# Kernel optimization log

Hardware: AMD Instinct MI355X
Metric: run time of the kernel (lower is better)

Reference implementation:

```python
import jax, jax.numpy as jnp
import numpy as np


def sparse_conv3d(images, kernel, default_value, base_plane, dilations=(1, 1, 1)):
    """Sparse 3D conv over a per-pixel base-plane-aligned volume.

    images:     [B, H, W, D, C]  local depth slabs per pixel
    kernel:     [kh, kw, kd, C, F]
    base_plane: [B, H, W, 1] int  global depth offset of slab start per pixel
    Neighbor sample at pixel (h', w') and local depth d uses that neighbor's
    local index d + od + base_plane[h,w] - base_plane[h',w']; out-of-range
    (spatial or depth) samples are filled with default_value.
    """
    B, H, W, D, C = images.shape
    kh, kw, kd, _, F = kernel.shape
    d0, d1, d2 = dilations
    bp = base_plane[..., 0].astype(jnp.int32)  # [B,H,W]
    hs = jnp.arange(H)
    ws = jnp.arange(W)
    ds = jnp.arange(D)
    dv = jnp.asarray(default_value, images.dtype).reshape(())
    out = jnp.zeros((B, H, W, D, F), images.dtype)
    for i in range(kh):
        oh = (i - kh // 2) * d0
        h_idx = hs + oh
        valid_h = (h_idx >= 0) & (h_idx < H)
        h_c = jnp.clip(h_idx, 0, H - 1)
        for j in range(kw):
            ow = (j - kw // 2) * d1
            w_idx = ws + ow
            valid_w = (w_idx >= 0) & (w_idx < W)
            w_c = jnp.clip(w_idx, 0, W - 1)
            # gather shifted neighbor slabs and their base offsets
            img_n = images[:, h_c][:, :, w_c]      # [B,H,W,D,C]
            bp_n = bp[:, h_c][:, :, w_c]            # [B,H,W]
            rel = (bp - bp_n)[..., None]            # depth realignment [B,H,W,1]
            sp_valid = (valid_h[None, :, None, None] & valid_w[None, None, :, None])
            for k in range(kd):
                od = (k - kd // 2) * d2
                d_idx = ds[None, None, None, :] + od + rel  # [B,H,W,D]
                valid = sp_valid & (d_idx >= 0) & (d_idx < D)
                d_c = jnp.clip(d_idx, 0, D - 1)
                vals = jnp.take_along_axis(img_n, d_c[..., None], axis=3)  # [B,H,W,D,C]
                vals = jnp.where(valid[..., None], vals, dv)
                out = out + jnp.einsum('bhwdc,cf->bhwdf', vals, kernel[i, j, k])
    return out


def setup_inputs() -> dict:
    key = jax.random.key(0)
    k1, k2, k3 = jax.random.split(key, 3)
    B, H, W, D, C, F = 2, 96, 128, 32, 16, 16
    images = jax.random.normal(k1, (B, H, W, D, C), dtype=jnp.float32)
    base_plane = jax.random.randint(k2, (B, H, W, 1), 0, 8, dtype=jnp.int32)
    kernel = jax.random.normal(k3, (3, 3, 3, C, F), dtype=jnp.float32) * 0.05
    default_value = jnp.zeros((1,), dtype=jnp.float32)
    return {"images": images, "base_plane": base_plane, "kernel": kernel,
            "default_value": default_value}


def reference(images, base_plane, kernel, default_value):
    return sparse_conv3d(images, kernel, default_value[0], base_plane, dilations=(1, 1, 1))
```

## Files before the change

### kernel.cpp

```cpp
#include <hip/hip_runtime.h>
#include <hip/hip_bf16.h>

typedef __attribute__((ext_vector_type(8))) short short8;
typedef __attribute__((ext_vector_type(4))) short s16x4;
typedef __attribute__((ext_vector_type(4))) float f32x4;
typedef __attribute__((ext_vector_type(4))) int i32x4;

#define NB_H 96
#define NB_W 128
#define NB_D 32
#define NB_C 16
#define NB_F 16
#define NPIX (2 * NB_H * NB_W)
#define KB2_U16 (14 * 512)
#define WS_NEED ((size_t)KB2_U16 * 2)
#define SLAB_STRIDE 1280
#define NSLAB 36
#define DV_OFF (NSLAB * SLAB_STRIDE)
#define KB_OFF (DV_OFF + 64)
#define LDS_BYTES (KB_OFF + KB2_U16 * 2)

static __device__ __forceinline__ short fcvt(float f) {
  return (short)__builtin_bit_cast(unsigned short, __float2bfloat16(f));
}


__global__ __launch_bounds__(256) void sconv3d_wprep(
    const float* __restrict__ kern, unsigned short* __restrict__ kb2) {
  const int i = blockIdx.x * 256 + threadIdx.x;
  if (i >= KB2_U16) return;
  const int p = i >> 9;
  const int g = (i >> 7) & 3;
  const int f = (i >> 3) & 15;
  const int j = i & 7;
  const int k = g * 8 + j;
  int lo, hi;
  if (p < 12) {
    const int q = p / 3, m = p % 3;
    lo = (m == 0) ? 6 * q : (m == 1) ? 6 * q + 3 : 6 * q + 2;
    hi = (m == 0) ? 6 * q + 1 : (m == 1) ? 6 * q + 4 : 6 * q + 5;
  } else if (p == 12) { lo = 24; hi = 25; }
  else { lo = 26; hi = -1; }
  const int t = (k < 16) ? lo : hi;
  const int c = k & 15;
  kb2[i] = (t >= 0) ? (unsigned short)fcvt(kern[(t * 16 + c) * 16 + f])
                    : (unsigned short)0;
}

__global__ __launch_bounds__(512, 4) void sconv3d_fused3(
    const float* __restrict__ img, const int* __restrict__ bp,
    const unsigned short* __restrict__ kb2, const float* __restrict__ dvp,
    float* __restrict__ out) {
  __shared__ char Sb[LDS_BYTES];
  const int tid = threadIdx.x;
  const int lane = tid & 63;
  const int r = lane & 15;
  const int grp = lane >> 4;
  const int vc = (grp & 1) * 16;
  const int halfbit = grp >> 1;
  const int rA = r + halfbit - 1;
  const int rX = r + 1;
  const int voff_dv = DV_OFF + vc;

  {
    const i32x4* src = (const i32x4*)kb2;
    i32x4* dst = (i32x4*)(Sb + KB_OFF);
    for (int i = tid; i < (KB2_U16 * 2) / 16; i += 512) dst[i] = src[i];
  }
  if (tid < 16) ((unsigned short*)(Sb + DV_OFF))[tid] =
      (unsigned short)fcvt(dvp[0]);

  const int bid = (blockIdx.x & 7) * 192 + (blockIdx.x >> 3);
  const int b = bid >= 768;
  const int rem = bid - b * 768;
  const int h0 = (rem >> 5) * 4;
  const int w0 = (rem & 31) * 4;

  const int t2 = tid & 127;
  const int sg = tid >> 7;
  const int srow = t2 >> 2;
  const int sb8 = (t2 & 3) * 8;
#pragma unroll
  for (int pass = 0; pass < 9; ++pass) {
    const int s = pass * 4 + sg;
    const int dh = s / 6, dw = s - 6 * dh;
    const int hh = min(max(h0 + dh - 1, 0), NB_H - 1);
    const int ww = min(max(w0 + dw - 1, 0), NB_W - 1);
    const float4 v = *(const float4*)(
        img + ((b * NB_H + hh) * NB_W + ww) * (NB_D * NB_C) + t2 * 4);
    s16x4 o;
    o[0] = fcvt(v.x); o[1] = fcvt(v.y); o[2] = fcvt(v.z); o[3] = fcvt(v.w);
    *(s16x4*)(Sb + s * SLAB_STRIDE + srow * 40 + sb8) = o;
  }

  const int wid = __builtin_amdgcn_readfirstlane((int)(tid >> 6));
  const int pw = wid & 3;
  const int phA = wid >> 2;
  const int phB = phA + 2;
  const int hA = h0 + phA, hB = h0 + phB, w = w0 + pw;
  const int pixA = (b * NB_H + hA) * NB_W + w;
  const int pixB = (b * NB_H + hB) * NB_W + w;
  const int bpcA = bp[pixA];
  const int bpcB = bp[pixB];

#define CALCN(PH, H, BPC, DI, DJ, SV, BA, RE)                           \
  {                                                                     \
    const int hh = (H) + (DI), ww = w + (DJ);                           \
    SV = (hh >= 0) & (hh < NB_H) & (ww >= 0) & (ww < NB_W);             \
    const int hc = min(max(hh, 0), NB_H - 1);                           \
    const int wc = min(max(ww, 0), NB_W - 1);                           \
    RE = (BPC)-bp[(b * NB_H + hc) * NB_W + wc];                         \
    BA = (((PH) + (DI) + 1) * 6 + pw + (DJ) + 1) * SLAB_STRIDE;         \
  }

  int Asv0, Aba0, Are0, Asv1, Aba1, Are1, Asv2, Aba2, Are2;
  int Asv3, Aba3, Are3, Asv4, Aba4, Are4, Asv5, Aba5, Are5;
  int Asv6, Aba6, Are6, Asv7, Aba7, Are7, Asv8, Aba8, Are8;
  int Bsv0, Bba0, Bre0, Bsv1, Bba1, Bre1, Bsv2, Bba2, Bre2;
  int Bsv3, Bba3, Bre3, Bsv4, Bba4, Bre4, Bsv5, Bba5, Bre5;
  int Bsv6, Bba6, Bre6, Bsv7, Bba7, Bre7, Bsv8, Bba8, Bre8;
  CALCN(phA, hA, bpcA, -1, -1, Asv0, Aba0, Are0);
  CALCN(phA, hA, bpcA, -1, 0, Asv1, Aba1, Are1);
  CALCN(phA, hA, bpcA, -1, 1, Asv2, Aba2, Are2);
  CALCN(phA, hA, bpcA, 0, -1, Asv3, Aba3, Are3);
  CALCN(phA, hA, bpcA, 0, 0, Asv4, Aba4, Are4);
  CALCN(phA, hA, bpcA, 0, 1, Asv5, Aba5, Are5);
  CALCN(phA, hA, bpcA, 1, -1, Asv6, Aba6, Are6);
  CALCN(phA, hA, bpcA, 1, 0, Asv7, Aba7, Are7);
  CALCN(phA, hA, bpcA, 1, 1, Asv8, Aba8, Are8);
  CALCN(phB, hB, bpcB, -1, -1, Bsv0, Bba0, Bre0);
  CALCN(phB, hB, bpcB, -1, 0, Bsv1, Bba1, Bre1);
  CALCN(phB, hB, bpcB, -1, 1, Bsv2, Bba2, Bre2);
  CALCN(phB, hB, bpcB, 0, -1, Bsv3, Bba3, Bre3);
  CALCN(phB, hB, bpcB, 0, 0, Bsv4, Bba4, Bre4);
  CALCN(phB, hB, bpcB, 0, 1, Bsv5, Bba5, Bre5);
  CALCN(phB, hB, bpcB, 1, -1, Bsv6, Bba6, Bre6);
  CALCN(phB, hB, bpcB, 1, 0, Bsv7, Bba7, Bre7);
  CALCN(phB, hB, bpcB, 1, 1, Bsv8, Bba8, Bre8);
#undef CALCN

  __syncthreads();

  f32x4 accA0 = {0.f, 0.f, 0.f, 0.f}, accA1 = {0.f, 0.f, 0.f, 0.f};
  f32x4 accB0 = {0.f, 0.f, 0.f, 0.f}, accB1 = {0.f, 0.f, 0.f, 0.f};

#define HALF(P, ROWBASE, SV, BA, RE, AC0, AC1, BF)                      \
  {                                                                     \
    const int ds0 = (ROWBASE) + (RE);                                   \
    int vo0 = (BA) + ds0 * 40 + vc;                                     \
    vo0 = ((SV) && (unsigned)ds0 < NB_D) ? vo0 : voff_dv;               \
    const short8 a0 = *(const short8*)(Sb + vo0);                       \
    AC0 = __builtin_amdgcn_mfma_f32_16x16x32_bf16(a0, BF, AC0, 0, 0, 0); \
    const int ds1 = ds0 + 16;                                           \
    int vo1 = (BA) + ds1 * 40 + vc;                                     \
    vo1 = ((SV) && (unsigned)ds1 < NB_D) ? vo1 : voff_dv;               \
    const short8 a1 = *(const short8*)(Sb + vo1);                       \
    AC1 = __builtin_amdgcn_mfma_f32_16x16x32_bf16(a1, BF, AC1, 0, 0, 0); \
  }

#define PAIR_UNIF(P, N)                                                 \
  {                                                                     \
    const short8 bf = *(const short8*)(Sb + KB_OFF + (P) * 1024 +       \
                                       grp * 256 + r * 16);             \
    HALF(P, rA, Asv##N, Aba##N, Are##N, accA0, accA1, bf);              \
    HALF(P, rA, Bsv##N, Bba##N, Bre##N, accB0, accB1, bf);              \
  }

#define PAIR_MIX(P, NE, NO)                                             \
  {                                                                     \
    const short8 bf = *(const short8*)(Sb + KB_OFF + (P) * 1024 +       \
                                       grp * 256 + r * 16);             \
    const int AsvS = halfbit ? Asv##NO : Asv##NE;                       \
    const int AbaS = halfbit ? Aba##NO : Aba##NE;                       \
    const int AreS = halfbit ? Are##NO : Are##NE;                       \
    HALF(P, rX, AsvS, AbaS, AreS, accA0, accA1, bf);                    \
    const int BsvS = halfbit ? Bsv##NO : Bsv##NE;                       \
    const int BbaS = halfbit ? Bba##NO : Bba##NE;                       \
    const int BreS = halfbit ? Bre##NO : Bre##NE;                       \
    HALF(P, rX, BsvS, BbaS, BreS, accB0, accB1, bf);                    \
  }

#define PAIR_MIX13(P, NE)                                               \
  {                                                                     \
    const short8 bf = *(const short8*)(Sb + KB_OFF + (P) * 1024 +       \
                                       grp * 256 + r * 16);             \
    const int AsvS = halfbit ? 0 : Asv##NE;                             \
    const int AbaS = Aba##NE;                                           \
    const int AreS = Are##NE;                                           \
    HALF(P, rX, AsvS, AbaS, AreS, accA0, accA1, bf);                    \
    const int BsvS = halfbit ? 0 : Bsv##NE;                             \
    const int BbaS = Bba##NE;                                           \
    const int BreS = Bre##NE;                                           \
    HALF(P, rX, BsvS, BbaS, BreS, accB0, accB1, bf);                    \
  }

  PAIR_UNIF(0, 0);
  PAIR_UNIF(1, 1);
  PAIR_MIX(2, 0, 1);
  PAIR_UNIF(3, 2);
  PAIR_UNIF(4, 3);
  PAIR_MIX(5, 2, 3);
  PAIR_UNIF(6, 4);
  PAIR_UNIF(7, 5);
  PAIR_MIX(8, 4, 5);
  PAIR_UNIF(9, 6);
  PAIR_UNIF(10, 7);
  PAIR_MIX(11, 6, 7);
  PAIR_UNIF(12, 8);
  PAIR_MIX13(13, 8);

#undef HALF
#undef PAIR_UNIF
#undef PAIR_MIX
#undef PAIR_MIX13

  const int obaseA = pixA * (NB_D * NB_F);
  const int obaseB = pixB * (NB_D * NB_F);
#pragma unroll
  for (int rr = 0; rr < 4; ++rr) {
    out[obaseA + (grp * 4 + rr) * NB_F + r] = accA0[rr];
    out[obaseA + (grp * 4 + rr + 16) * NB_F + r] = accA1[rr];
    out[obaseB + (grp * 4 + rr) * NB_F + r] = accB0[rr];
    out[obaseB + (grp * 4 + rr + 16) * NB_F + r] = accB1[rr];
  }
}

__global__ __launch_bounds__(256) void sconv3d_mfma(
    const float* __restrict__ img, const int* __restrict__ bp,
    const float* __restrict__ kern, const float* __restrict__ dvp,
    float* __restrict__ out, int npix) {
  __shared__ unsigned short Kb[28 * 256];
  const int tid = threadIdx.x;
  for (int idx = tid; idx < 28 * 256; idx += 256) {
    unsigned short v = 0;
    if (idx < 27 * 256) v = (unsigned short)fcvt(kern[idx]);
    Kb[idx] = v;
  }
  __syncthreads();

  const int lane = tid & 63;
  const int grp = lane >> 4;
  const int r = lane & 15;
  const int c0 = (grp & 1) * 8;
  const int half = grp >> 1;

  short8 bfrag[14];
#pragma unroll
  for (int p = 0; p < 14; ++p) {
#pragma unroll
    for (int j = 0; j < 8; ++j) {
      const int k = 8 * grp + j;
      const int t = 2 * p + (k >> 4);
      bfrag[p][j] = (short)Kb[t * 256 + (k & 15) * 16 + r];
    }
  }

  const int pix = blockIdx.x * 4 + (tid >> 6);
  if (pix >= npix) return;
  const int b = pix / (NB_H * NB_W);
  const int rem = pix - b * (NB_H * NB_W);
  const int h = rem >> 7;
  const int w = rem & (NB_W - 1);

  const float dv = dvp[0];
  const int bpc = bp[pix];

  f32x4 acc0 = {0.f, 0.f, 0.f, 0.f};
  f32x4 acc1 = {0.f, 0.f, 0.f, 0.f};

#pragma unroll
  for (int p = 0; p < 14; ++p) {
    const int t = 2 * p + half;
    const int n = t / 3;
    const int kd = t - 3 * n;
    const int i = n / 3;
    const int j = n - 3 * i;
    const int hh = h + i - 1;
    const int ww = w + j - 1;
    const bool sv =
        (t < 27) && (hh >= 0) && (hh < NB_H) && (ww >= 0) && (ww < NB_W);
    const int hc = min(max(hh, 0), NB_H - 1);
    const int wc = min(max(ww, 0), NB_W - 1);
    const int nidx = (b * NB_H + hc) * NB_W + wc;
    const int rel = bpc - bp[nidx];
    const int base = nidx * (NB_D * NB_C);
    const int dsh = (kd - 1) + rel;

    const int ds0 = r + dsh;
    short8 a0;
    {
      float va[8];
      if (sv && (ds0 >= 0) && (ds0 < NB_D)) {
        const float4* pp = (const float4*)(img + base + ds0 * NB_C + c0);
        const float4 x = pp[0];
        const float4 y = pp[1];
        va[0] = x.x; va[1] = x.y; va[2] = x.z; va[3] = x.w;
        va[4] = y.x; va[5] = y.y; va[6] = y.z; va[7] = y.w;
      } else {
#pragma unroll
        for (int q = 0; q < 8; ++q) va[q] = dv;
      }
#pragma unroll
      for (int q = 0; q < 8; ++q) a0[q] = fcvt(va[q]);
    }
    acc0 = __builtin_amdgcn_mfma_f32_16x16x32_bf16(a0, bfrag[p], acc0, 0, 0, 0);

    const int ds1 = ds0 + 16;
    short8 a1;
    {
      float va[8];
      if (sv && (ds1 >= 0) && (ds1 < NB_D)) {
        const float4* pp = (const float4*)(img + base + ds1 * NB_C + c0);
        const float4 x = pp[0];
        const float4 y = pp[1];
        va[0] = x.x; va[1] = x.y; va[2] = x.z; va[3] = x.w;
        va[4] = y.x; va[5] = y.y; va[6] = y.z; va[7] = y.w;
      } else {
#pragma unroll
        for (int q = 0; q < 8; ++q) va[q] = dv;
      }
#pragma unroll
      for (int q = 0; q < 8; ++q) a1[q] = fcvt(va[q]);
    }
    acc1 = __builtin_amdgcn_mfma_f32_16x16x32_bf16(a1, bfrag[p], acc1, 0, 0, 0);
  }

  const int obase = pix * (NB_D * NB_F);
#pragma unroll
  for (int rr = 0; rr < 4; ++rr) {
    out[obase + (grp * 4 + rr) * NB_F + r] = acc0[rr];
    out[obase + (grp * 4 + rr + 16) * NB_F + r] = acc1[rr];
  }
}

extern "C" void kernel_launch(void* const* d_in, const int* in_sizes, int n_in,
                              void* d_out, int out_size, void* d_ws, size_t ws_size,
                              hipStream_t stream) {
  const float* img = (const float*)d_in[0];
  const int* bp = (const int*)d_in[1];
  const float* kern = (const float*)d_in[2];
  const float* dvp = (const float*)d_in[3];
  float* out = (float*)d_out;

  if (ws_size >= WS_NEED) {
    unsigned short* kb2 = (unsigned short*)d_ws;
    sconv3d_wprep<<<28, 256, 0, stream>>>(kern, kb2);
    sconv3d_fused3<<<NPIX / 16, 512, 0, stream>>>(img, bp, kb2, dvp, out);
  } else {
    sconv3d_mfma<<<NPIX / 4, 256, 0, stream>>>(img, bp, kern, dvp, out, NPIX);
  }
}
```

Measured before the change: 49.52 us.

## Shrink block tile to 2x4 pixels, keep weights in registers, software-pipeline LDS loads

Each block now covers a 2x4 pixel tile with 256 threads instead of a 4x4 tile with 512, so the halo shrinks from 36 to 24 slabs. The bf16 weight fragments are loaded from global straight into registers instead of being staged in LDS. The MFMA loop is reordered to double-buffer the A-operand LDS loads (X/Y sets), so loads for the next tap overlap the MFMAs of the current one. In exchange the halo-to-output ratio is worse, so more redundant global image reads and bf16 conversions per output, and register pressure rises from the 14 weight fragments plus the double buffers.

```diff
diff --git a/kernel.cpp b/kernel.cpp
--- a/kernel.cpp
+++ b/kernel.cpp
@@ -4,7 +4,6 @@
 typedef __attribute__((ext_vector_type(8))) short short8;
 typedef __attribute__((ext_vector_type(4))) short s16x4;
 typedef __attribute__((ext_vector_type(4))) float f32x4;
-typedef __attribute__((ext_vector_type(4))) int i32x4;
 
 #define NB_H 96
 #define NB_W 128
@@ -15,10 +14,9 @@
 #define KB2_U16 (14 * 512)
 #define WS_NEED ((size_t)KB2_U16 * 2)
 #define SLAB_STRIDE 1280
-#define NSLAB 36
+#define NSLAB 24
 #define DV_OFF (NSLAB * SLAB_STRIDE)
-#define KB_OFF (DV_OFF + 64)
-#define LDS_BYTES (KB_OFF + KB2_U16 * 2)
+#define LDS_BYTES (DV_OFF + 64)
 
 static __device__ __forceinline__ short fcvt(float f) {
   return (short)__builtin_bit_cast(unsigned short, __float2bfloat16(f));
@@ -47,7 +45,7 @@
                     : (unsigned short)0;
 }
 
-__global__ __launch_bounds__(512, 4) void sconv3d_fused3(
+__global__ __launch_bounds__(256, 4) void sconv3d_fused4(
     const float* __restrict__ img, const int* __restrict__ bp,
     const unsigned short* __restrict__ kb2, const float* __restrict__ dvp,
     float* __restrict__ out) {
@@ -62,18 +60,15 @@
   const int rX = r + 1;
   const int voff_dv = DV_OFF + vc;
 
-  {
-    const i32x4* src = (const i32x4*)kb2;
-    i32x4* dst = (i32x4*)(Sb + KB_OFF);
-    for (int i = tid; i < (KB2_U16 * 2) / 16; i += 512) dst[i] = src[i];
-  }
-  if (tid < 16) ((unsigned short*)(Sb + DV_OFF))[tid] =
-      (unsigned short)fcvt(dvp[0]);
-
-  const int bid = (blockIdx.x & 7) * 192 + (blockIdx.x >> 3);
-  const int b = bid >= 768;
-  const int rem = bid - b * 768;
-  const int h0 = (rem >> 5) * 4;
+  short8 bfrag[14];
+#pragma unroll
+  for (int p = 0; p < 14; ++p)
+    bfrag[p] = *(const short8*)(kb2 + p * 512 + grp * 128 + r * 8);
+
+  const int bid = (blockIdx.x & 7) * 384 + (blockIdx.x >> 3);
+  const int b = bid >= 1536;
+  const int rem = bid - b * 1536;
+  const int h0 = (rem >> 5) * 2;
   const int w0 = (rem & 31) * 4;
 
   const int t2 = tid & 127;
@@ -81,8 +76,8 @@
   const int srow = t2 >> 2;
   const int sb8 = (t2 & 3) * 8;
 #pragma unroll
-  for (int pass = 0; pass < 9; ++pass) {
-    const int s = pass * 4 + sg;
+  for (int pass = 0; pass < 12; ++pass) {
+    const int s = pass * 2 + sg;
     const int dh = s / 6, dw = s - 6 * dh;
     const int hh = min(max(h0 + dh - 1, 0), NB_H - 1);
     const int ww = min(max(w0 + dw - 1, 0), NB_W - 1);
@@ -92,14 +87,14 @@
     o[0] = fcvt(v.x); o[1] = fcvt(v.y); o[2] = fcvt(v.z); o[3] = fcvt(v.w);
     *(s16x4*)(Sb + s * SLAB_STRIDE + srow * 40 + sb8) = o;
   }
+  if (tid < 16) ((unsigned short*)(Sb + DV_OFF))[tid] =
+      (unsigned short)fcvt(dvp[0]);
 
   const int wid = __builtin_amdgcn_readfirstlane((int)(tid >> 6));
-  const int pw = wid & 3;
-  const int phA = wid >> 2;
-  const int phB = phA + 2;
-  const int hA = h0 + phA, hB = h0 + phB, w = w0 + pw;
+  const int w = w0 + wid;
+  const int hA = h0, hB = h0 + 1;
   const int pixA = (b * NB_H + hA) * NB_W + w;
-  const int pixB = (b * NB_H + hB) * NB_W + w;
+  const int pixB = pixA + NB_W;
   const int bpcA = bp[pixA];
   const int bpcB = bp[pixB];
 
@@ -110,7 +105,7 @@
     const int hc = min(max(hh, 0), NB_H - 1);                           \
     const int wc = min(max(ww, 0), NB_W - 1);                           \
     RE = (BPC)-bp[(b * NB_H + hc) * NB_W + wc];                         \
-    BA = (((PH) + (DI) + 1) * 6 + pw + (DJ) + 1) * SLAB_STRIDE;         \
+    BA = (((PH) + (DI) + 1) * 6 + wid + (DJ) + 1) * SLAB_STRIDE;        \
   }
 
   int Asv0, Aba0, Are0, Asv1, Aba1, Are1, Asv2, Aba2, Are2;
@@ -119,24 +114,24 @@
   int Bsv0, Bba0, Bre0, Bsv1, Bba1, Bre1, Bsv2, Bba2, Bre2;
   int Bsv3, Bba3, Bre3, Bsv4, Bba4, Bre4, Bsv5, Bba5, Bre5;
   int Bsv6, Bba6, Bre6, Bsv7, Bba7, Bre7, Bsv8, Bba8, Bre8;
-  CALCN(phA, hA, bpcA, -1, -1, Asv0, Aba0, Are0);
-  CALCN(phA, hA, bpcA, -1, 0, Asv1, Aba1, Are1);
-  CALCN(phA, hA, bpcA, -1, 1, Asv2, Aba2, Are2);
-  CALCN(phA, hA, bpcA, 0, -1, Asv3, Aba3, Are3);
-  CALCN(phA, hA, bpcA, 0, 0, Asv4, Aba4, Are4);
-  CALCN(phA, hA, bpcA, 0, 1, Asv5, Aba5, Are5);
-  CALCN(phA, hA, bpcA, 1, -1, Asv6, Aba6, Are6);
-  CALCN(phA, hA, bpcA, 1, 0, Asv7, Aba7, Are7);
-  CALCN(phA, hA, bpcA, 1, 1, Asv8, Aba8, Are8);
-  CALCN(phB, hB, bpcB, -1, -1, Bsv0, Bba0, Bre0);
-  CALCN(phB, hB, bpcB, -1, 0, Bsv1, Bba1, Bre1);
-  CALCN(phB, hB, bpcB, -1, 1, Bsv2, Bba2, Bre2);
-  CALCN(phB, hB, bpcB, 0, -1, Bsv3, Bba3, Bre3);
-  CALCN(phB, hB, bpcB, 0, 0, Bsv4, Bba4, Bre4);
-  CALCN(phB, hB, bpcB, 0, 1, Bsv5, Bba5, Bre5);
-  CALCN(phB, hB, bpcB, 1, -1, Bsv6, Bba6, Bre6);
-  CALCN(phB, hB, bpcB, 1, 0, Bsv7, Bba7, Bre7);
-  CALCN(phB, hB, bpcB, 1, 1, Bsv8, Bba8, Bre8);
+  CALCN(0, hA, bpcA, -1, -1, Asv0, Aba0, Are0);
+  CALCN(0, hA, bpcA, -1, 0, Asv1, Aba1, Are1);
+  CALCN(0, hA, bpcA, -1, 1, Asv2, Aba2, Are2);
+  CALCN(0, hA, bpcA, 0, -1, Asv3, Aba3, Are3);
+  CALCN(0, hA, bpcA, 0, 0, Asv4, Aba4, Are4);
+  CALCN(0, hA, bpcA, 0, 1, Asv5, Aba5, Are5);
+  CALCN(0, hA, bpcA, 1, -1, Asv6, Aba6, Are6);
+  CALCN(0, hA, bpcA, 1, 0, Asv7, Aba7, Are7);
+  CALCN(0, hA, bpcA, 1, 1, Asv8, Aba8, Are8);
+  CALCN(1, hB, bpcB, -1, -1, Bsv0, Bba0, Bre0);
+  CALCN(1, hB, bpcB, -1, 0, Bsv1, Bba1, Bre1);
+  CALCN(1, hB, bpcB, -1, 1, Bsv2, Bba2, Bre2);
+  CALCN(1, hB, bpcB, 0, -1, Bsv3, Bba3, Bre3);
+  CALCN(1, hB, bpcB, 0, 0, Bsv4, Bba4, Bre4);
+  CALCN(1, hB, bpcB, 0, 1, Bsv5, Bba5, Bre5);
+  CALCN(1, hB, bpcB, 1, -1, Bsv6, Bba6, Bre6);
+  CALCN(1, hB, bpcB, 1, 0, Bsv7, Bba7, Bre7);
+  CALCN(1, hB, bpcB, 1, 1, Bsv8, Bba8, Bre8);
 #undef CALCN
 
   __syncthreads();
@@ -144,75 +139,77 @@
   f32x4 accA0 = {0.f, 0.f, 0.f, 0.f}, accA1 = {0.f, 0.f, 0.f, 0.f};
   f32x4 accB0 = {0.f, 0.f, 0.f, 0.f}, accB1 = {0.f, 0.f, 0.f, 0.f};
 
-#define HALF(P, ROWBASE, SV, BA, RE, AC0, AC1, BF)                      \
-  {                                                                     \
-    const int ds0 = (ROWBASE) + (RE);                                   \
-    int vo0 = (BA) + ds0 * 40 + vc;                                     \
-    vo0 = ((SV) && (unsigned)ds0 < NB_D) ? vo0 : voff_dv;               \
-    const short8 a0 = *(const short8*)(Sb + vo0);                       \
-    AC0 = __builtin_amdgcn_mfma_f32_16x16x32_bf16(a0, BF, AC0, 0, 0, 0); \
-    const int ds1 = ds0 + 16;                                           \
-    int vo1 = (BA) + ds1 * 40 + vc;                                     \
-    vo1 = ((SV) && (unsigned)ds1 < NB_D) ? vo1 : voff_dv;               \
-    const short8 a1 = *(const short8*)(Sb + vo1);                       \
-    AC1 = __builtin_amdgcn_mfma_f32_16x16x32_bf16(a1, BF, AC1, 0, 0, 0); \
-  }
-
-#define PAIR_UNIF(P, N)                                                 \
-  {                                                                     \
-    const short8 bf = *(const short8*)(Sb + KB_OFF + (P) * 1024 +       \
-                                       grp * 256 + r * 16);             \
-    HALF(P, rA, Asv##N, Aba##N, Are##N, accA0, accA1, bf);              \
-    HALF(P, rA, Bsv##N, Bba##N, Bre##N, accB0, accB1, bf);              \
-  }
-
-#define PAIR_MIX(P, NE, NO)                                             \
-  {                                                                     \
-    const short8 bf = *(const short8*)(Sb + KB_OFF + (P) * 1024 +       \
-                                       grp * 256 + r * 16);             \
-    const int AsvS = halfbit ? Asv##NO : Asv##NE;                       \
-    const int AbaS = halfbit ? Aba##NO : Aba##NE;                       \
-    const int AreS = halfbit ? Are##NO : Are##NE;                       \
-    HALF(P, rX, AsvS, AbaS, AreS, accA0, accA1, bf);                    \
-    const int BsvS = halfbit ? Bsv##NO : Bsv##NE;                       \
-    const int BbaS = halfbit ? Bba##NO : Bba##NE;                       \
-    const int BreS = halfbit ? Bre##NO : Bre##NE;                       \
-    HALF(P, rX, BsvS, BbaS, BreS, accB0, accB1, bf);                    \
-  }
-
-#define PAIR_MIX13(P, NE)                                               \
-  {                                                                     \
-    const short8 bf = *(const short8*)(Sb + KB_OFF + (P) * 1024 +       \
-                                       grp * 256 + r * 16);             \
-    const int AsvS = halfbit ? 0 : Asv##NE;                             \
-    const int AbaS = Aba##NE;                                           \
-    const int AreS = Are##NE;                                           \
-    HALF(P, rX, AsvS, AbaS, AreS, accA0, accA1, bf);                    \
-    const int BsvS = halfbit ? 0 : Bsv##NE;                             \
-    const int BbaS = Bba##NE;                                           \
-    const int BreS = Bre##NE;                                           \
-    HALF(P, rX, BsvS, BbaS, BreS, accB0, accB1, bf);                    \
-  }
-
-  PAIR_UNIF(0, 0);
-  PAIR_UNIF(1, 1);
-  PAIR_MIX(2, 0, 1);
-  PAIR_UNIF(3, 2);
-  PAIR_UNIF(4, 3);
-  PAIR_MIX(5, 2, 3);
-  PAIR_UNIF(6, 4);
-  PAIR_UNIF(7, 5);
-  PAIR_MIX(8, 4, 5);
-  PAIR_UNIF(9, 6);
-  PAIR_UNIF(10, 7);
-  PAIR_MIX(11, 6, 7);
-  PAIR_UNIF(12, 8);
-  PAIR_MIX13(13, 8);
-
-#undef HALF
-#undef PAIR_UNIF
-#undef PAIR_MIX
-#undef PAIR_MIX13
+  short8 Xa0, Xa1, Xb0, Xb1, Ya0, Ya1, Yb0, Yb1;
+
+#define LOADQ(S, DS0A, BAA, SVA, DS0B, BAB, SVB)                        \
+  {                                                                     \
+    int d_, o_;                                                         \
+    d_ = (DS0A);      o_ = (BAA) + d_ * 40 + vc;                        \
+    o_ = ((SVA) && (unsigned)d_ < NB_D) ? o_ : voff_dv;                 \
+    S##a0 = *(const short8*)(Sb + o_);                                  \
+    d_ = (DS0A) + 16; o_ = (BAA) + d_ * 40 + vc;                        \
+    o_ = ((SVA) && (unsigned)d_ < NB_D) ? o_ : voff_dv;                 \
+    S##a1 = *(const short8*)(Sb + o_);                                  \
+    d_ = (DS0B);      o_ = (BAB) + d_ * 40 + vc;                        \
+    o_ = ((SVB) && (unsigned)d_ < NB_D) ? o_ : voff_dv;                 \
+    S##b0 = *(const short8*)(Sb + o_);                                  \
+    d_ = (DS0B) + 16; o_ = (BAB) + d_ * 40 + vc;                        \
+    o_ = ((SVB) && (unsigned)d_ < NB_D) ? o_ : voff_dv;                 \
+    S##b1 = *(const short8*)(Sb + o_);                                  \
+  }
+
+#define LOAD_U(S, N) \
+  LOADQ(S, rA + Are##N, Aba##N, Asv##N, rA + Bre##N, Bba##N, Bsv##N)
+
+#define LOAD_M(S, NE, NO)                                               \
+  {                                                                     \
+    const int asv = halfbit ? Asv##NO : Asv##NE;                        \
+    const int aba = halfbit ? Aba##NO : Aba##NE;                        \
+    const int are = halfbit ? Are##NO : Are##NE;                        \
+    const int bsv = halfbit ? Bsv##NO : Bsv##NE;                        \
+    const int bba = halfbit ? Bba##NO : Bba##NE;                        \
+    const int bre = halfbit ? Bre##NO : Bre##NE;                        \
+    LOADQ(S, rX + are, aba, asv, rX + bre, bba, bsv)                    \
+  }
+
+#define LOAD_M13(S, NE)                                                 \
+  {                                                                     \
+    const int asv = halfbit ? 0 : Asv##NE;                              \
+    const int bsv = halfbit ? 0 : Bsv##NE;                              \
+    LOADQ(S, rX + Are##NE, Aba##NE, asv, rX + Bre##NE, Bba##NE, bsv)    \
+  }
+
+#define FMA4(P, S)                                                      \
+  {                                                                     \
+    const short8 bf = bfrag[P];                                         \
+    accA0 = __builtin_amdgcn_mfma_f32_16x16x32_bf16(S##a0, bf, accA0, 0, 0, 0); \
+    accA1 = __builtin_amdgcn_mfma_f32_16x16x32_bf16(S##a1, bf, accA1, 0, 0, 0); \
+    accB0 = __builtin_amdgcn_mfma_f32_16x16x32_bf16(S##b0, bf, accB0, 0, 0, 0); \
+    accB1 = __builtin_amdgcn_mfma_f32_16x16x32_bf16(S##b1, bf, accB1, 0, 0, 0); \
+  }
+
+  LOAD_U(X, 0);
+  LOAD_U(Y, 1);
+  FMA4(0, X);  LOAD_M(X, 0, 1);
+  FMA4(1, Y);  LOAD_U(Y, 2);
+  FMA4(2, X);  LOAD_U(X, 3);
+  FMA4(3, Y);  LOAD_M(Y, 2, 3);
+  FMA4(4, X);  LOAD_U(X, 4);
+  FMA4(5, Y);  LOAD_U(Y, 5);
+  FMA4(6, X);  LOAD_M(X, 4, 5);
+  FMA4(7, Y);  LOAD_U(Y, 6);
+  FMA4(8, X);  LOAD_U(X, 7);
+  FMA4(9, Y);  LOAD_M(Y, 6, 7);
+  FMA4(10, X); LOAD_U(X, 8);
+  FMA4(11, Y); LOAD_M13(Y, 8);
+  FMA4(12, X);
+  FMA4(13, Y);
+
+#undef LOADQ
+#undef LOAD_U
+#undef LOAD_M
+#undef LOAD_M13
+#undef FMA4
 
   const int obaseA = pixA * (NB_D * NB_F);
   const int obaseB = pixB * (NB_D * NB_F);
@@ -345,7 +342,7 @@
   if (ws_size >= WS_NEED) {
     unsigned short* kb2 = (unsigned short*)d_ws;
     sconv3d_wprep<<<28, 256, 0, stream>>>(kern, kb2);
-    sconv3d_fused3<<<NPIX / 16, 512, 0, stream>>>(img, bp, kb2, dvp, out);
+    sconv3d_fused4<<<NPIX / 8, 256, 0, stream>>>(img, bp, kb2, dvp, out);
   } else {
     sconv3d_mfma<<<NPIX / 4, 256, 0, stream>>>(img, bp, kern, dvp, out, NPIX);
   }
```

Measured after the change: 47.17 us. 4.8% less time.
